# Kernel optimization log

Hardware: AMD Instinct MI355X
Metric: run time of the kernel (lower is better)

Reference implementation:

```python
import jax, jax.numpy as jnp
import numpy as np


def setup_inputs() -> dict:
    key = jax.random.key(0)
    k1, k2 = jax.random.split(key)
    B, C, H, W = 16, 128, 32, 32   # C == embedding_dim
    K = 2048                        # codebook size (num_embeddings)
    x = jax.random.normal(k1, (B, C, H, W), dtype=jnp.float32)
    codebook = jax.random.normal(k2, (K, C), dtype=jnp.float32)
    return {"x": x, "codebook": codebook}


def reference(x, codebook):
    # x: [B, C, H, W] -> NHWC -> flatten to [N, C]
    B, C, H, W = x.shape
    x_nhwc = jnp.transpose(x, (0, 2, 3, 1))
    x_flat = x_nhwc.reshape(-1, C)                      # [N, C]
    # Squared L2 distances via expansion (argmin-equivalent to torch.norm
    # of the broadcast difference, without the [N, K, C] intermediate):
    x_sq = jnp.sum(x_flat * x_flat, axis=1, keepdims=True)   # [N, 1]
    w_sq = jnp.sum(codebook * codebook, axis=1)              # [K]
    d2 = x_sq - 2.0 * (x_flat @ codebook.T) + w_sq           # [N, K]
    encoding_indices = jnp.argmin(d2, axis=1)                # [N]
    encodings = jax.nn.one_hot(encoding_indices, codebook.shape[0],
                               dtype=x_flat.dtype)           # [N, K]
    quantized = encodings @ codebook                         # [N, C]
    quantized = jnp.transpose(quantized.reshape(B, H, W, C), (0, 3, 1, 2))
    return encodings, quantized
```

## Files before the change

### kernel.cpp

```cpp
#include <hip/hip_runtime.h>
#include <hip/hip_bf16.h>

#define N_TOK  16384
#define KCODES 2048
#define CDIM   128
#define BM     32
#define TPB    256
#define NCW    4
#define CPW    (KCODES / NCW)
#define TPW    (CPW / 16)
#define SEEDT  8
#define CAP    128
#define DELTA  5.0f
#define ASTR   36

typedef __attribute__((ext_vector_type(8))) short bhalf8;
typedef __attribute__((ext_vector_type(4))) float facc4;

__global__ __launch_bounds__(256) void prep_kernel(const float* __restrict__ cb,
                                                   bhalf8* __restrict__ cbt,
                                                   float* __restrict__ wsq) {
    const int T   = blockIdx.x;
    const int tid = threadIdx.x;
    const int r   = tid >> 4;
    const int g   = tid & 15;
    const float4* src = (const float4*)(cb + ((size_t)(T * 16 + r)) * CDIM + g * 8);
    float4 a0 = src[0], a1 = src[1];

    float s = a0.x*a0.x + a0.y*a0.y + a0.z*a0.z + a0.w*a0.w
            + a1.x*a1.x + a1.y*a1.y + a1.z*a1.z + a1.w*a1.w;
    s += __shfl_xor(s, 1, 64);
    s += __shfl_xor(s, 2, 64);
    s += __shfl_xor(s, 4, 64);
    s += __shfl_xor(s, 8, 64);
    if (g == 0) wsq[T * 16 + r] = s;

    union { unsigned u[4]; bhalf8 v; } fu;
    __hip_bfloat162 h0 = __float22bfloat162_rn(make_float2(a0.x, a0.y));
    __hip_bfloat162 h1 = __float22bfloat162_rn(make_float2(a0.z, a0.w));
    __hip_bfloat162 h2 = __float22bfloat162_rn(make_float2(a1.x, a1.y));
    __hip_bfloat162 h3 = __float22bfloat162_rn(make_float2(a1.z, a1.w));
    fu.u[0] = *(unsigned*)&h0; fu.u[1] = *(unsigned*)&h1;
    fu.u[2] = *(unsigned*)&h2; fu.u[3] = *(unsigned*)&h3;
    const int kf = g >> 2, q = g & 3;
    cbt[(size_t)T * 256 + kf * 64 + q * 16 + r] = fu.v;
}

__global__ __launch_bounds__(TPB, 2) void argmin_kernel(const float* __restrict__ x,
                                                        const float* __restrict__ cb,
                                                        const bhalf8* __restrict__ cbt,
                                                        const float* __restrict__ wsqg,
                                                        float* __restrict__ enc,
                                                        float* __restrict__ quant) {
    __shared__ float As[CDIM][ASTR];
    __shared__ float wsqs[KCODES];
    __shared__ float redvw[NCW][BM];
    __shared__ float rowthr[BM];
    __shared__ int   cnt[BM];
    __shared__ int   candk[BM][CAP];
    __shared__ int   rowidx[BM];

    const int tid  = threadIdx.x;
    const int lane = tid & 63;
    const int w    = tid >> 6;
    const int q    = lane >> 4;
    const int r    = lane & 15;
    const int n0   = blockIdx.x * BM;
    const int b    = n0 >> 10;
    const int hw0  = n0 & 1023;

    {
        int m4 = (tid & 7) << 2;
        int c0 = tid >> 3;
        #pragma unroll
        for (int i = 0; i < 4; i++) {
            int c = c0 + 32 * i;
            float4 v = *(const float4*)(x + (((size_t)(b * CDIM + c)) << 10) + hw0 + m4);
            *(float4*)(&As[c][m4]) = v;
        }
    }
    #pragma unroll
    for (int i = 0; i < KCODES / TPB; i++) wsqs[i * TPB + tid] = wsqg[i * TPB + tid];
    if (tid < BM) cnt[tid] = 0;
    __syncthreads();

    bhalf8 af[2][4];
    #pragma unroll
    for (int rt = 0; rt < 2; rt++) {
        int m = rt * 16 + r;
        #pragma unroll
        for (int kf = 0; kf < 4; kf++) {
            union { unsigned u[4]; bhalf8 v; } fu;
            #pragma unroll
            for (int p = 0; p < 4; p++) {
                int k = kf * 32 + q * 8 + 2 * p;
                __hip_bfloat162 h = __float22bfloat162_rn(make_float2(As[k][m], As[k + 1][m]));
                fu.u[p] = *(unsigned*)&h;
            }
            af[rt][kf] = fu.v;
        }
    }

    const int    cw  = w * CPW;
    const size_t tb0 = (size_t)(cw >> 4) * 256;

    {
        float rmin[8];
        #pragma unroll
        for (int t = 0; t < 8; t++) rmin[t] = 3.0e38f;

        for (int t = 0; t < SEEDT; t++) {
            bhalf8 bt[4];
            #pragma unroll
            for (int kf = 0; kf < 4; kf++) bt[kf] = cbt[tb0 + (size_t)t * 256 + kf * 64 + lane];
            facc4 acc[2];
            #pragma unroll
            for (int rt = 0; rt < 2; rt++) acc[rt] = (facc4){0.f, 0.f, 0.f, 0.f};
            #pragma unroll
            for (int kf = 0; kf < 4; kf++)
                #pragma unroll
                for (int rt = 0; rt < 2; rt++)
                    acc[rt] = __builtin_amdgcn_mfma_f32_16x16x32_bf16(af[rt][kf], bt[kf], acc[rt], 0, 0, 0);
            float wv = wsqs[cw + t * 16 + r];
            #pragma unroll
            for (int rt = 0; rt < 2; rt++)
                #pragma unroll
                for (int i = 0; i < 4; i++)
                    rmin[rt * 4 + i] = fminf(rmin[rt * 4 + i], fmaf(-2.f, acc[rt][i], wv));
        }
        #pragma unroll
        for (int t = 0; t < 8; t++) {
            float v = rmin[t];
            v = fminf(v, __shfl_xor(v, 1, 64));
            v = fminf(v, __shfl_xor(v, 2, 64));
            v = fminf(v, __shfl_xor(v, 4, 64));
            v = fminf(v, __shfl_xor(v, 8, 64));
            if (r == 0) redvw[w][(t >> 2) * 16 + q * 4 + (t & 3)] = v;
        }
    }
    __syncthreads();
    if (tid < BM) {
        float mv = fminf(fminf(redvw[0][tid], redvw[1][tid]),
                         fminf(redvw[2][tid], redvw[3][tid]));
        rowthr[tid] = mv + DELTA;
    }
    __syncthreads();

    {
        float thr[8];
        #pragma unroll
        for (int t = 0; t < 8; t++) thr[t] = rowthr[(t >> 2) * 16 + q * 4 + (t & 3)];

        bhalf8 bcur[4], bnxt[4];
        #pragma unroll
        for (int kf = 0; kf < 4; kf++) bcur[kf] = cbt[tb0 + kf * 64 + lane];
        #pragma unroll
        for (int kf = 0; kf < 4; kf++) bnxt[kf] = cbt[tb0 + 256 + kf * 64 + lane];

        for (int t = 0; t < TPW; t++) {
            bhalf8 bn2[4];
            if (t + 2 < TPW) {
                size_t tb = tb0 + (size_t)(t + 2) * 256;
                #pragma unroll
                for (int kf = 0; kf < 4; kf++) bn2[kf] = cbt[tb + kf * 64 + lane];
            }
            facc4 acc[2];
            #pragma unroll
            for (int rt = 0; rt < 2; rt++) acc[rt] = (facc4){0.f, 0.f, 0.f, 0.f};
            #pragma unroll
            for (int kf = 0; kf < 4; kf++)
                #pragma unroll
                for (int rt = 0; rt < 2; rt++)
                    acc[rt] = __builtin_amdgcn_mfma_f32_16x16x32_bf16(af[rt][kf], bcur[kf], acc[rt], 0, 0, 0);
            float wv = wsqs[cw + t * 16 + r];
            #pragma unroll
            for (int rt = 0; rt < 2; rt++)
                #pragma unroll
                for (int i = 0; i < 4; i++) {
                    float d = fmaf(-2.f, acc[rt][i], wv);
                    if (d <= thr[rt * 4 + i]) {
                        int row = rt * 16 + q * 4 + i;
                        int p = atomicAdd(&cnt[row], 1);
                        if (p < CAP) candk[row][p] = cw + t * 16 + r;
                    }
                }
            #pragma unroll
            for (int kf = 0; kf < 4; kf++) { bcur[kf] = bnxt[kf]; bnxt[kf] = bn2[kf]; }
        }
    }
    __syncthreads();

    for (int m = 8 * w; m < 8 * w + 8; m++) {
        int c = cnt[m];
        float bv = 3.0e38f; int bk = 0x7fffffff;
        if (c > CAP) {
            for (int k = lane; k < KCODES; k += 64) {
                float s = 0.f;
                for (int cd = 0; cd < CDIM; cd++)
                    s = fmaf(As[cd][m], cb[(size_t)k * CDIM + cd], s);
                float d = fmaf(-2.f, s, wsqs[k]);
                if (d < bv || (d == bv && k < bk)) { bv = d; bk = k; }
            }
            #pragma unroll
            for (int off = 1; off <= 32; off <<= 1) {
                float ov = __shfl_xor(bv, off, 64);
                int   ok = __shfl_xor(bk, off, 64);
                if (ov < bv || (ov == bv && ok < bk)) { bv = ov; bk = ok; }
            }
        } else {
            for (int t = 0; t < c; t++) {
                int k = candk[m][t];
                float x0 = As[lane][m], x1 = As[lane + 64][m];
                float c0 = cb[(size_t)k * CDIM + lane];
                float c1 = cb[(size_t)k * CDIM + 64 + lane];
                float s = x0 * c0 + x1 * c1;
                #pragma unroll
                for (int off = 1; off <= 32; off <<= 1) s += __shfl_xor(s, off, 64);
                float d = fmaf(-2.f, s, wsqs[k]);
                if (d < bv || (d == bv && k < bk)) { bv = d; bk = k; }
            }
        }
        if (bk == 0x7fffffff) bk = 0;
        if (lane == 0) rowidx[m] = bk;
    }
    __syncthreads();

    if (tid < BM) enc[(size_t)(n0 + tid) * KCODES + rowidx[tid]] = 1.0f;

    #pragma unroll
    for (int i = tid; i < BM * CDIM / 4; i += TPB) {
        int c  = i >> 3;
        int hq = (i & 7) << 2;
        float4 v;
        v.x = cb[(size_t)rowidx[hq + 0] * CDIM + c];
        v.y = cb[(size_t)rowidx[hq + 1] * CDIM + c];
        v.z = cb[(size_t)rowidx[hq + 2] * CDIM + c];
        v.w = cb[(size_t)rowidx[hq + 3] * CDIM + c];
        *(float4*)(quant + (((size_t)(b * CDIM + c)) << 10) + hw0 + hq) = v;
    }
}

extern "C" void kernel_launch(void* const* d_in, const int* in_sizes, int n_in,
                              void* d_out, int out_size, void* d_ws, size_t ws_size,
                              hipStream_t stream) {
    const float* x  = (const float*)d_in[0];
    const float* cb = (const float*)d_in[1];
    float* out = (float*)d_out;

    bhalf8* cbt  = (bhalf8*)d_ws;
    float*  wsqp = (float*)((char*)d_ws + 512 * 1024);

    hipMemsetAsync(out, 0, (size_t)N_TOK * KCODES * sizeof(float), stream);
    prep_kernel<<<KCODES / 16, 256, 0, stream>>>(cb, cbt, wsqp);
    argmin_kernel<<<N_TOK / BM, TPB, 0, stream>>>(x, cb, cbt, wsqp,
                                                  out, out + (size_t)N_TOK * KCODES);
}
```

Baseline: 230.5 us.

## Fuse one-hot zeroing into argmin kernel and halve the row tile

```diff
diff --git a/kernel.cpp b/kernel.cpp
--- a/kernel.cpp
+++ b/kernel.cpp
@@ -4,15 +4,15 @@
 #define N_TOK  16384
 #define KCODES 2048
 #define CDIM   128
-#define BM     32
+#define BM     16
 #define TPB    256
 #define NCW    4
 #define CPW    (KCODES / NCW)
 #define TPW    (CPW / 16)
 #define SEEDT  8
-#define CAP    128
+#define CAP    64
 #define DELTA  5.0f
-#define ASTR   36
+#define ASTR   20
 
 typedef __attribute__((ext_vector_type(8))) short bhalf8;
 typedef __attribute__((ext_vector_type(4))) float facc4;
@@ -46,7 +46,7 @@
     cbt[(size_t)T * 256 + kf * 64 + q * 16 + r] = fu.v;
 }
 
-__global__ __launch_bounds__(TPB, 2) void argmin_kernel(const float* __restrict__ x,
+__global__ __launch_bounds__(TPB, 4) void argmin_kernel(const float* __restrict__ x,
                                                         const float* __restrict__ cb,
                                                         const bhalf8* __restrict__ cbt,
                                                         const float* __restrict__ wsqg,
@@ -68,13 +68,14 @@
     const int n0   = blockIdx.x * BM;
     const int b    = n0 >> 10;
     const int hw0  = n0 & 1023;
-
-    {
-        int m4 = (tid & 7) << 2;
-        int c0 = tid >> 3;
-        #pragma unroll
-        for (int i = 0; i < 4; i++) {
-            int c = c0 + 32 * i;
+    const float4 z4 = {0.f, 0.f, 0.f, 0.f};
+
+    {
+        int m4 = (tid & 3) << 2;
+        int c0 = tid >> 2;
+        #pragma unroll
+        for (int i = 0; i < 2; i++) {
+            int c = c0 + 64 * i;
             float4 v = *(const float4*)(x + (((size_t)(b * CDIM + c)) << 10) + hw0 + m4);
             *(float4*)(&As[c][m4]) = v;
         }
@@ -84,10 +85,9 @@
     if (tid < BM) cnt[tid] = 0;
     __syncthreads();
 
-    bhalf8 af[2][4];
-    #pragma unroll
-    for (int rt = 0; rt < 2; rt++) {
-        int m = rt * 16 + r;
+    bhalf8 af[4];
+    {
+        int m = r;
         #pragma unroll
         for (int kf = 0; kf < 4; kf++) {
             union { unsigned u[4]; bhalf8 v; } fu;
@@ -97,7 +97,7 @@
                 __hip_bfloat162 h = __float22bfloat162_rn(make_float2(As[k][m], As[k + 1][m]));
                 fu.u[p] = *(unsigned*)&h;
             }
-            af[rt][kf] = fu.v;
+            af[kf] = fu.v;
         }
     }
 
@@ -105,37 +105,31 @@
     const size_t tb0 = (size_t)(cw >> 4) * 256;
 
     {
-        float rmin[8];
-        #pragma unroll
-        for (int t = 0; t < 8; t++) rmin[t] = 3.0e38f;
+        float rmin[4];
+        #pragma unroll
+        for (int t = 0; t < 4; t++) rmin[t] = 3.0e38f;
 
         for (int t = 0; t < SEEDT; t++) {
             bhalf8 bt[4];
             #pragma unroll
             for (int kf = 0; kf < 4; kf++) bt[kf] = cbt[tb0 + (size_t)t * 256 + kf * 64 + lane];
-            facc4 acc[2];
-            #pragma unroll
-            for (int rt = 0; rt < 2; rt++) acc[rt] = (facc4){0.f, 0.f, 0.f, 0.f};
+            facc4 acc = (facc4){0.f, 0.f, 0.f, 0.f};
             #pragma unroll
             for (int kf = 0; kf < 4; kf++)
-                #pragma unroll
-                for (int rt = 0; rt < 2; rt++)
-                    acc[rt] = __builtin_amdgcn_mfma_f32_16x16x32_bf16(af[rt][kf], bt[kf], acc[rt], 0, 0, 0);
+                acc = __builtin_amdgcn_mfma_f32_16x16x32_bf16(af[kf], bt[kf], acc, 0, 0, 0);
             float wv = wsqs[cw + t * 16 + r];
             #pragma unroll
-            for (int rt = 0; rt < 2; rt++)
-                #pragma unroll
-                for (int i = 0; i < 4; i++)
-                    rmin[rt * 4 + i] = fminf(rmin[rt * 4 + i], fmaf(-2.f, acc[rt][i], wv));
-        }
-        #pragma unroll
-        for (int t = 0; t < 8; t++) {
+            for (int i = 0; i < 4; i++)
+                rmin[i] = fminf(rmin[i], fmaf(-2.f, acc[i], wv));
+        }
+        #pragma unroll
+        for (int t = 0; t < 4; t++) {
             float v = rmin[t];
             v = fminf(v, __shfl_xor(v, 1, 64));
             v = fminf(v, __shfl_xor(v, 2, 64));
             v = fminf(v, __shfl_xor(v, 4, 64));
             v = fminf(v, __shfl_xor(v, 8, 64));
-            if (r == 0) redvw[w][(t >> 2) * 16 + q * 4 + (t & 3)] = v;
+            if (r == 0) redvw[w][q * 4 + t] = v;
         }
     }
     __syncthreads();
@@ -147,9 +141,11 @@
     __syncthreads();
 
     {
-        float thr[8];
-        #pragma unroll
-        for (int t = 0; t < 8; t++) thr[t] = rowthr[(t >> 2) * 16 + q * 4 + (t & 3)];
+        float thr[4];
+        #pragma unroll
+        for (int t = 0; t < 4; t++) thr[t] = rowthr[q * 4 + t];
+
+        float4* fdst = (float4*)(enc + (size_t)n0 * KCODES);
 
         bhalf8 bcur[4], bnxt[4];
         #pragma unroll
@@ -164,33 +160,28 @@
                 #pragma unroll
                 for (int kf = 0; kf < 4; kf++) bn2[kf] = cbt[tb + kf * 64 + lane];
             }
-            facc4 acc[2];
-            #pragma unroll
-            for (int rt = 0; rt < 2; rt++) acc[rt] = (facc4){0.f, 0.f, 0.f, 0.f};
+            fdst[t * TPB + tid] = z4;
+            facc4 acc = (facc4){0.f, 0.f, 0.f, 0.f};
             #pragma unroll
             for (int kf = 0; kf < 4; kf++)
-                #pragma unroll
-                for (int rt = 0; rt < 2; rt++)
-                    acc[rt] = __builtin_amdgcn_mfma_f32_16x16x32_bf16(af[rt][kf], bcur[kf], acc[rt], 0, 0, 0);
+                acc = __builtin_amdgcn_mfma_f32_16x16x32_bf16(af[kf], bcur[kf], acc, 0, 0, 0);
             float wv = wsqs[cw + t * 16 + r];
             #pragma unroll
-            for (int rt = 0; rt < 2; rt++)
-                #pragma unroll
-                for (int i = 0; i < 4; i++) {
-                    float d = fmaf(-2.f, acc[rt][i], wv);
-                    if (d <= thr[rt * 4 + i]) {
-                        int row = rt * 16 + q * 4 + i;
-                        int p = atomicAdd(&cnt[row], 1);
-                        if (p < CAP) candk[row][p] = cw + t * 16 + r;
-                    }
+            for (int i = 0; i < 4; i++) {
+                float d = fmaf(-2.f, acc[i], wv);
+                if (d <= thr[i]) {
+                    int row = q * 4 + i;
+                    int p = atomicAdd(&cnt[row], 1);
+                    if (p < CAP) candk[row][p] = cw + t * 16 + r;
                 }
+            }
             #pragma unroll
             for (int kf = 0; kf < 4; kf++) { bcur[kf] = bnxt[kf]; bnxt[kf] = bn2[kf]; }
         }
     }
     __syncthreads();
 
-    for (int m = 8 * w; m < 8 * w + 8; m++) {
+    for (int m = 4 * w; m < 4 * w + 4; m++) {
         int c = cnt[m];
         float bv = 3.0e38f; int bk = 0x7fffffff;
         if (c > CAP) {
@@ -229,8 +220,8 @@
 
     #pragma unroll
     for (int i = tid; i < BM * CDIM / 4; i += TPB) {
-        int c  = i >> 3;
-        int hq = (i & 7) << 2;
+        int c  = i >> 2;
+        int hq = (i & 3) << 2;
         float4 v;
         v.x = cb[(size_t)rowidx[hq + 0] * CDIM + c];
         v.y = cb[(size_t)rowidx[hq + 1] * CDIM + c];
@@ -250,7 +241,6 @@
     bhalf8* cbt  = (bhalf8*)d_ws;
     float*  wsqp = (float*)((char*)d_ws + 512 * 1024);
 
-    hipMemsetAsync(out, 0, (size_t)N_TOK * KCODES * sizeof(float), stream);
     prep_kernel<<<KCODES / 16, 256, 0, stream>>>(cb, cbt, wsqp);
     argmin_kernel<<<N_TOK / BM, TPB, 0, stream>>>(x, cb, cbt, wsqp,
                                                   out, out + (size_t)N_TOK * KCODES);
```

Result: faster. 199.1 us (-13.6%).
